# Optimization experiments

Measured on AMD Instinct MI355X. Metric: run time of the kernel, lower is better.

Reference implementation:

```python
import jax, jax.numpy as jnp
import numpy as np

# quantization / activation scales (stand-ins for act_scales dict entries)
S_IN = 0.05      # in_proj:input
S_Z = 0.02       # in_proj:output (also gate/z scale)
S_U = 0.01       # x_proj:input (conv output scale)
S_DTLN = 0.02    # dt_layernorm:output
S_B = 0.02       # B_layernorm:output
S_C = 0.02       # C_layernorm:output
S_DT = 0.01      # dt_proj:output
S_Y = 0.01       # out_proj:input
EPS = 1e-6
R = 128          # time_step_rank
N = 16           # ssm_state_size


def qa(x, s):
    # simulate int8 activation quantization (values kept in fp32)
    return jnp.clip(jnp.round(x / s), -128.0, 127.0)


def qw(w):
    # per-tensor symmetric int8 weight quantization
    s = jnp.max(jnp.abs(w)) / 127.0
    return jnp.clip(jnp.round(w / s), -128.0, 127.0), s


def rmsnorm_q(x, w, s):
    x = x.astype(jnp.float32)
    x = x * jax.lax.rsqrt(jnp.mean(x * x, axis=-1, keepdims=True) + EPS)
    return qa(w * x, s)


def ssm_scan(u, dt, A, Bm, Cm):
    # u, dt: [B, D, S]; Bm, Cm: [B, S, N]; A: [D, N]
    def step(h, xs):
        dt_t, u_t, B_t, C_t = xs                     # [B,D],[B,D],[B,N],[B,N]
        dA = jnp.exp(dt_t[..., None] * A)            # [B,D,N]
        h = h * dA + (dt_t * u_t)[..., None] * B_t[:, None, :]
        y = jnp.einsum('bdn,bn->bd', h, C_t)
        return h, y
    Bsz, Dd, S = u.shape
    h0 = jnp.zeros((Bsz, Dd, A.shape[1]), u.dtype)
    xs = (jnp.moveaxis(dt, 2, 0), jnp.moveaxis(u, 2, 0),
          jnp.moveaxis(Bm, 1, 0), jnp.moveaxis(Cm, 1, 0))
    _, ys = jax.lax.scan(step, h0, xs)               # ys: [S,B,D]
    return jnp.moveaxis(ys, 0, 2)                    # [B,D,S]


def setup_inputs() -> dict:
    key = jax.random.key(0)
    ks = jax.random.split(key, 10)
    B, S, H, Din, K = 2, 2048, 2048, 4096, 4
    return {
        'hidden_states': jax.random.normal(ks[0], (B, S, H), jnp.float32),
        'in_proj_w': jax.random.normal(ks[1], (2 * Din, H), jnp.float32) * 0.02,
        'conv_w': jax.random.normal(ks[2], (Din, K), jnp.float32) * 0.1,
        'conv_b': jax.random.normal(ks[3], (Din,), jnp.float32) * 0.01,
        'x_proj_w': jax.random.normal(ks[4], (R + 2 * N, Din), jnp.float32) * 0.02,
        'dt_ln_w': jnp.ones((R,), jnp.float32),
        'B_ln_w': jnp.ones((N,), jnp.float32),
        'C_ln_w': jnp.ones((N,), jnp.float32),
        'dt_proj_w': jax.random.normal(ks[5], (Din, R), jnp.float32) * 0.05,
        'dt_bias': jax.random.normal(ks[6], (Din,), jnp.float32) * 0.5 - 4.0,
        'A_log': jnp.log(jnp.broadcast_to(jnp.arange(1, N + 1, dtype=jnp.float32), (Din, N))),
        'D_skip': jnp.ones((Din,), jnp.float32),
        'out_proj_w': jax.random.normal(ks[7], (H, Din), jnp.float32) * 0.02,
    }


def reference(hidden_states, in_proj_w, conv_w, conv_b, x_proj_w, dt_ln_w,
              B_ln_w, C_ln_w, dt_proj_w, dt_bias, A_log, D_skip, out_proj_w):
    # --- in_proj (W8A8B8O8), then seqlen-last layout [B, 2D, S] ---
    x_q = qa(hidden_states, S_IN)
    wq, ws = qw(in_proj_w)
    proj_q = qa((x_q @ wq.T) * (S_IN * ws), S_Z)          # [B,S,2D] int8-valued
    proj_q = jnp.swapaxes(proj_q, 1, 2)                   # [B,2D,S]
    Din = proj_q.shape[1] // 2
    hs_q, gate_q = proj_q[:, :Din], proj_q[:, Din:]

    # --- quantized causal depthwise conv1d + silu (QCausalConv1D) ---
    cwq, cws = qw(conv_w)
    K = conv_w.shape[1]
    conv_out = jax.lax.conv_general_dilated(
        hs_q, cwq[:, None, :], (1,), [(K - 1, 0)],
        dimension_numbers=('NCH', 'OIH', 'NCH'), feature_group_count=Din)
    conv_out = conv_out * (S_Z * cws) + conv_b[None, :, None]
    u_q = qa(jax.nn.silu(conv_out), S_U)                  # [B,Din,S]

    # --- x_proj (W8A8BF16OF16) -> dt/B/C, inner RMSNorms + quant ---
    xwq, xws = qw(x_proj_w)
    ssm_p = (jnp.swapaxes(u_q, 1, 2) @ xwq.T) * (S_U * xws)   # [B,S,R+2N] float
    dt_q = rmsnorm_q(ssm_p[..., :R], dt_ln_w, S_DTLN)
    B_q = rmsnorm_q(ssm_p[..., R:R + N], B_ln_w, S_B)
    C_q = rmsnorm_q(ssm_p[..., R + N:], C_ln_w, S_C)

    # --- dt_proj (W8A8B8O8, bias folded into scan) ---
    dwq, dws = qw(dt_proj_w)
    dt8 = qa((dt_q @ dwq.T) * (S_DTLN * dws), S_DT)       # [B,S,Din]
    dt = jax.nn.softplus(jnp.swapaxes(dt8, 1, 2) * S_DT + dt_bias[None, :, None])

    # --- selective scan (QSScan): dequantize, recur, gate ---
    u = u_q * S_U
    A = -jnp.exp(A_log)
    ys = ssm_scan(u, dt, A, B_q * S_B, C_q * S_C)         # [B,Din,S]
    ys = ys + u * D_skip[None, :, None]
    ys = ys * jax.nn.silu(gate_q * S_Z)

    # --- QAct + out_proj (W8A8BF16OF16) ---
    y_q = qa(jnp.swapaxes(ys, 1, 2), S_Y)                 # [B,S,Din]
    owq, ows = qw(out_proj_w)
    return (y_q @ owq.T) * (S_Y * ows)                    # [B,S,H]
```

## Files before the change

### kernel.cpp

```cpp
#include <hip/hip_runtime.h>
#include <stdint.h>

typedef signed char i8;
typedef int v4i __attribute__((ext_vector_type(4)));

#define S_IN  0.05f
#define S_Z   0.02f
#define S_U   0.01f
#define S_DTLN 0.02f
#define S_B   0.02f
#define S_C   0.02f
#define S_DT  0.01f
#define S_Y   0.01f

__device__ __forceinline__ float q8f(float x, float s) {
    float r = rintf(x / s);
    return fmaxf(-128.0f, fminf(127.0f, r));
}
__device__ __forceinline__ int q8i(float x, float s) { return (int)q8f(x, s); }

__device__ __forceinline__ float softplus_f(float x) {
    return __fadd_rn(fmaxf(x, 0.0f), log1pf(expf(-fabsf(x))));
}

__device__ __forceinline__ int sbyte_of(int w, int j) {
    return (int)(signed char)((unsigned)w >> (j * 8));
}
__device__ __forceinline__ int ubyte_of(int w, int j) {
    return (int)(((unsigned)w >> (j * 8)) & 255u);
}

__device__ __forceinline__ void gload16(const i8* g, i8* lds) {
    __builtin_amdgcn_global_load_lds(
        (const __attribute__((address_space(1))) unsigned int*)g,
        (__attribute__((address_space(3))) unsigned int*)lds,
        16, 0, 0);
}

__global__ __launch_bounds__(256)
void k_maxabs_all(const float* __restrict__ a0, const float* __restrict__ a1,
                  const float* __restrict__ a2, const float* __restrict__ a3,
                  const float* __restrict__ a4, unsigned* __restrict__ out) {
    int bid = blockIdx.x;
    const float* w; long long n; int slot, nb;
    if (bid < 2048)      { w = a0; n = 16777216LL; slot = 0; nb = 2048; }
    else if (bid < 2112) { w = a1; n = 16384LL;    slot = 1; nb = 64;   bid -= 2048; }
    else if (bid < 2624) { w = a2; n = 655360LL;   slot = 2; nb = 512;  bid -= 2112; }
    else if (bid < 3136) { w = a3; n = 524288LL;   slot = 3; nb = 512;  bid -= 2624; }
    else                 { w = a4; n = 8388608LL;  slot = 4; nb = 1024; bid -= 3136; }
    unsigned m = 0;
    long long stride = (long long)nb * 256;
    for (long long i = (long long)bid * 256 + threadIdx.x; i < n; i += stride)
        m = max(m, __float_as_uint(fabsf(w[i])));
    #pragma unroll
    for (int off = 32; off; off >>= 1) {
        unsigned o = (unsigned)__shfl_xor((int)m, off);
        m = max(m, o);
    }
    __shared__ unsigned sm[4];
    if ((threadIdx.x & 63) == 0) sm[threadIdx.x >> 6] = m;
    __syncthreads();
    if (threadIdx.x == 0) {
        unsigned r = max(max(sm[0], sm[1]), max(sm[2], sm[3]));
        atomicMax(out + slot, r);
    }
}

__global__ __launch_bounds__(256)
void k_quant_all(const float* __restrict__ a0, const float* __restrict__ a1,
                 const float* __restrict__ a2, const float* __restrict__ a3,
                 const float* __restrict__ a4, const float* __restrict__ ax,
                 const unsigned* __restrict__ scales,
                 i8* __restrict__ o0, i8* __restrict__ o1, i8* __restrict__ o2,
                 i8* __restrict__ o3, i8* __restrict__ o4, i8* __restrict__ ox) {
    int bid = blockIdx.x;
    const float* w; i8* o; float s;
    if (bid < 16384)      { w = a0; o = o0; s = __uint_as_float(scales[0]) / 127.0f; }
    else if (bid < 16400) { w = a1; o = o1; s = __uint_as_float(scales[1]) / 127.0f; bid -= 16384; }
    else if (bid < 17040) { w = a2; o = o2; s = __uint_as_float(scales[2]) / 127.0f; bid -= 16400; }
    else if (bid < 17552) { w = a3; o = o3; s = __uint_as_float(scales[3]) / 127.0f; bid -= 17040; }
    else if (bid < 25744) { w = a4; o = o4; s = __uint_as_float(scales[4]) / 127.0f; bid -= 17552; }
    else                  { w = ax; o = ox; s = S_IN;                                 bid -= 25744; }
    long long i = ((long long)bid * 256 + threadIdx.x) * 4;
    float4 v = *(const float4*)(w + i);
    unsigned pk = ((unsigned)(q8i(v.x, s) & 255))
                | ((unsigned)(q8i(v.y, s) & 255) << 8)
                | ((unsigned)(q8i(v.z, s) & 255) << 16)
                | ((unsigned)(q8i(v.w, s) & 255) << 24);
    *(unsigned*)(o + i) = pk;
}

template<int EPI>
__global__ __launch_bounds__(256)
void k_mgemm(const i8* __restrict__ A, const i8* __restrict__ Bw,
             int M, int N, int K,
             const unsigned* __restrict__ wmaxbits,
             void* __restrict__ out0, void* __restrict__ out1) {
    __shared__ i8 sA[16384];
    __shared__ i8 sB[16384];
    const int tid = threadIdx.x;
    const int w = tid >> 6;
    const int l = tid & 63;
    int id = blockIdx.y * gridDim.x + blockIdx.x;
    const int qq = (gridDim.x * gridDim.y) >> 3;
    id = (id & 7) * qq + (id >> 3);
    const int m0 = (id / gridDim.x) << 7;
    const int n0 = (id % gridDim.x) << 7;
    const int kLen = K / gridDim.z;
    const int kOff = blockIdx.z * kLen;
    const int lr = l & 15;
    const int lk = l >> 4;
    const i8* gA = A  + (size_t)(m0 + lr) * K + lk * 16;
    const i8* gB = Bw + (size_t)(n0 + lr) * K + lk * 16;
    const size_t rowK16 = (size_t)16 * K;
    const int mw = (w >> 1) * 4;
    const int nw = (w & 1) * 4;
    const int rdoff = lk * 256 + lr * 16;
    v4i acc[4][4] = {};
    for (int k0 = kOff; k0 < kOff + kLen; k0 += 128) {
        gload16(gA + rowK16 * w + k0,            sA + w * 2048);
        gload16(gA + rowK16 * w + k0 + 64,       sA + w * 2048 + 1024);
        gload16(gA + rowK16 * (4 + w) + k0,      sA + (4 + w) * 2048);
        gload16(gA + rowK16 * (4 + w) + k0 + 64, sA + (4 + w) * 2048 + 1024);
        gload16(gB + rowK16 * w + k0,            sB + w * 2048);
        gload16(gB + rowK16 * w + k0 + 64,       sB + w * 2048 + 1024);
        gload16(gB + rowK16 * (4 + w) + k0,      sB + (4 + w) * 2048);
        gload16(gB + rowK16 * (4 + w) + k0 + 64, sB + (4 + w) * 2048 + 1024);
        __syncthreads();
        #pragma unroll
        for (int k64 = 0; k64 < 2; k64++) {
            v4i af[4], bf[4];
            #pragma unroll
            for (int t = 0; t < 4; t++) {
                af[t] = *(const v4i*)(sA + (mw + t) * 2048 + k64 * 1024 + rdoff);
                bf[t] = *(const v4i*)(sB + (nw + t) * 2048 + k64 * 1024 + rdoff);
            }
            #pragma unroll
            for (int mt = 0; mt < 4; mt++)
                #pragma unroll
                for (int nt = 0; nt < 4; nt++)
                    acc[mt][nt] = __builtin_amdgcn_mfma_i32_16x16x64_i8(af[mt], bf[nt], acc[mt][nt], 0, 0, 0);
        }
        __syncthreads();
    }
    const float wsc = __uint_as_float(*wmaxbits) / 127.0f;
    const int m0w = m0 + (w >> 1) * 64;
    const int n0w = n0 + (w & 1) * 64;
    if constexpr (EPI == 0 || EPI == 2) {
        const float sc = (EPI == 0 ? S_IN : S_DTLN) * wsc;
        const float qs = (EPI == 0 ? S_Z : S_DT);
        const int b = m0w >> 11;
        #pragma unroll
        for (int nt = 0; nt < 4; nt++) {
            const int j = n0w + nt * 16 + lr;
            i8* dst;
            if constexpr (EPI == 0) dst = (j < 4096) ? (i8*)out0 : (i8*)out1;
            else dst = (i8*)out0;
            const int jj = j & 4095;
            #pragma unroll
            for (int mt = 0; mt < 4; mt++) {
                const int sbase = (m0w & 2047) + mt * 16 + lk * 4;
                unsigned pk = 0;
                #pragma unroll
                for (int r = 0; r < 4; r++) {
                    float v = (float)acc[mt][nt][r] * sc;
                    pk |= ((unsigned)(q8i(v, qs) & 255)) << (8 * r);
                }
                *(unsigned*)(dst + ((size_t)b * 4096 + jj) * 2048 + sbase) = pk;
            }
        }
    } else if constexpr (EPI == 1) {
        int* O = (int*)out0;
        #pragma unroll
        for (int mt = 0; mt < 4; mt++)
            #pragma unroll
            for (int r = 0; r < 4; r++) {
                const int m = m0w + mt * 16 + lk * 4 + r;
                #pragma unroll
                for (int nt = 0; nt < 4; nt++) {
                    const int j = n0w + nt * 16 + lr;
                    if (j < 160)
                        atomicAdd(O + (size_t)m * 160 + j, acc[mt][nt][r]);
                }
            }
    } else {
        const float sc = S_Y * wsc;
        float* O = (float*)out0;
        #pragma unroll
        for (int mt = 0; mt < 4; mt++)
            #pragma unroll
            for (int r = 0; r < 4; r++) {
                const int m = m0w + mt * 16 + lk * 4 + r;
                #pragma unroll
                for (int nt = 0; nt < 4; nt++)
                    O[(size_t)m * N + n0w + nt * 16 + lr] = (float)acc[mt][nt][r] * sc;
            }
    }
}

__global__ __launch_bounds__(256)
void k_conv(const i8* __restrict__ hsq, const i8* __restrict__ cwq,
            const float* __restrict__ conv_b, const unsigned* __restrict__ cmaxbits,
            i8* __restrict__ uq, i8* __restrict__ uqT) {
    __shared__ char lt[64][68];
    const int tid = threadIdx.x;
    const int b = blockIdx.z;
    const int d0 = blockIdx.y << 6;
    const int s0 = blockIdx.x << 6;
    const int dl = tid >> 2;
    const int sg = tid & 3;
    const int d = d0 + dl;
    const int sbase = s0 + (sg << 4);
    const i8* xp = hsq + ((size_t)b * 4096 + d) * 2048;
    int v[19];
    #pragma unroll
    for (int i = 0; i < 19; i++) {
        int s = sbase - 3 + i;
        v[i] = (s >= 0) ? (int)xp[s] : 0;
    }
    const unsigned cw = *(const unsigned*)(cwq + (size_t)d * 4);
    const int w0 = (int)(char)(cw & 255);
    const int w1 = (int)(char)((cw >> 8) & 255);
    const int w2 = (int)(char)((cw >> 16) & 255);
    const int w3 = (int)(char)((cw >> 24) & 255);
    const float cws = __uint_as_float(*cmaxbits) / 127.0f;
    const float sc = S_Z * cws;
    const float bias = conv_b[d];
    unsigned pk[4] = {0, 0, 0, 0};
    #pragma unroll
    for (int t = 0; t < 16; t++) {
        int acc = v[t] * w0 + v[t + 1] * w1 + v[t + 2] * w2 + v[t + 3] * w3;
        float f = __fadd_rn(__fmul_rn((float)acc, sc), bias);
        float sig = 1.0f / (1.0f + expf(-f));
        float sl = __fmul_rn(f, sig);
        int q = q8i(sl, S_U);
        pk[t >> 2] |= ((unsigned)(q & 255)) << ((t & 3) * 8);
        lt[(sg << 4) + t][dl] = (char)q;
    }
    *(int4*)(uq + ((size_t)b * 4096 + d) * 2048 + sbase) = make_int4(pk[0], pk[1], pk[2], pk[3]);
    __syncthreads();
    const int rr = tid >> 2;
    const int wg = tid & 3;
    const int* rp = (const int*)(&lt[rr][wg << 4]);
    int4 o; o.x = rp[0]; o.y = rp[1]; o.z = rp[2]; o.w = rp[3];
    *(int4*)(uqT + ((size_t)b * 2048 + s0 + rr) * 4096 + d0 + (wg << 4)) = o;
}

__global__ __launch_bounds__(64)
void k_rms(const int* __restrict__ p, const unsigned* __restrict__ xsc,
           const float* __restrict__ wdt, const float* __restrict__ wB, const float* __restrict__ wC,
           i8* __restrict__ dtq, i8* __restrict__ bqT, i8* __restrict__ cqT) {
    const int row = blockIdx.x;
    const int lane = threadIdx.x;
    const float scp = S_U * (__uint_as_float(*xsc) / 127.0f);
    const int* x = p + (size_t)row * 160;
    float a0 = (float)x[lane] * scp;
    float a1 = (float)x[64 + lane] * scp;
    float bb = (lane < 16) ? (float)x[128 + lane] * scp : 0.0f;
    float cc = (lane < 16) ? (float)x[144 + lane] * scp : 0.0f;
    float sdt = __fadd_rn(__fmul_rn(a0, a0), __fmul_rn(a1, a1));
    float sB = __fmul_rn(bb, bb);
    float sC = __fmul_rn(cc, cc);
    #pragma unroll
    for (int off = 32; off; off >>= 1) {
        sdt = __fadd_rn(sdt, __shfl_xor(sdt, off));
        sB  = __fadd_rn(sB,  __shfl_xor(sB, off));
        sC  = __fadd_rn(sC,  __shfl_xor(sC, off));
    }
    float rdt = 1.0f / sqrtf(sdt / 128.0f + 1e-6f);
    float rB  = 1.0f / sqrtf(sB / 16.0f + 1e-6f);
    float rC  = 1.0f / sqrtf(sC / 16.0f + 1e-6f);
    dtq[(size_t)row * 128 + lane]      = (i8)q8i(__fmul_rn(wdt[lane],      __fmul_rn(a0, rdt)), S_DTLN);
    dtq[(size_t)row * 128 + 64 + lane] = (i8)q8i(__fmul_rn(wdt[64 + lane], __fmul_rn(a1, rdt)), S_DTLN);
    if (lane < 16) {
        size_t tpos = ((size_t)(row >> 11) * 16 + lane) * 2048 + (row & 2047);
        bqT[tpos] = (i8)q8i(__fmul_rn(wB[lane], __fmul_rn(bb, rB)), S_B);
        cqT[tpos] = (i8)q8i(__fmul_rn(wC[lane], __fmul_rn(cc, rC)), S_C);
    }
}

__global__ __launch_bounds__(256)
void k_lut_all(const float* __restrict__ dt_bias, float* __restrict__ lutdt,
               float* __restrict__ lutsi) {
    const int q = threadIdx.x;
    const int sv = (q < 128) ? q : q - 256;
    if (blockIdx.x < 4096) {
        const int d = blockIdx.x;
        const float bias = dt_bias[d];
        lutdt[(size_t)d * 256 + q] =
            softplus_f(__fadd_rn(__fmul_rn((float)sv, S_DT), bias));
    } else {
        float gv = __fmul_rn((float)sv, S_Z);
        float sg = __fmul_rn(gv, 1.0f / (1.0f + expf(-gv)));
        lutsi[q] = sg;
    }
}

__global__ __launch_bounds__(256)
void k_scan4(const i8* __restrict__ dt8, const i8* __restrict__ uq, const i8* __restrict__ gq,
             const i8* __restrict__ BqT, const i8* __restrict__ CqT,
             const float* __restrict__ lut_dt, const float* __restrict__ lut_silu,
             const float* __restrict__ A_log, const float* __restrict__ D_skip,
             i8* __restrict__ yq) {
    const int g = blockIdx.x * 256 + threadIdx.x;
    const int n = g & 15;
    const int bd = g >> 4;
    const int d = bd & 4095;
    const int b = bd >> 12;
    const float Acoef = -expf(A_log[(size_t)d * 16 + n]);
    const float Dd = D_skip[d];
    const float* ldt = lut_dt + (size_t)d * 256;
    const v4i* dtp = (const v4i*)(dt8 + (size_t)bd * 2048);
    const v4i* up  = (const v4i*)(uq  + (size_t)bd * 2048);
    const v4i* gp  = (const v4i*)(gq  + (size_t)bd * 2048);
    const v4i* Bp  = (const v4i*)(BqT + ((size_t)b * 16 + n) * 2048);
    const v4i* Cp  = (const v4i*)(CqT + ((size_t)b * 16 + n) * 2048);
    i8* yp = yq + (size_t)b * 2048 * 4096 + d;
    float h = 0.0f;
    v4i dtw = dtp[0], uw = up[0], gw = gp[0], bw = Bp[0], cw = Cp[0];
    for (int t = 0; t < 128; t++) {
        v4i ndt, nu, ng, nb, nc;
        if (t < 127) { ndt = dtp[t + 1]; nu = up[t + 1]; ng = gp[t + 1]; nb = Bp[t + 1]; nc = Cp[t + 1]; }
        float dtv[16], dA[16], pj[16], Cv[16], y[16];
        #pragma unroll
        for (int j = 0; j < 16; j++)
            dtv[j] = ldt[ubyte_of(dtw[j >> 2], j & 3)];
        #pragma unroll
        for (int j = 0; j < 16; j++)
            dA[j] = expf(__fmul_rn(dtv[j], Acoef));
        #pragma unroll
        for (int j = 0; j < 16; j++) {
            float uv = __fmul_rn((float)sbyte_of(uw[j >> 2], j & 3), S_U);
            float Bv = __fmul_rn((float)sbyte_of(bw[j >> 2], j & 3), S_B);
            Cv[j] = __fmul_rn((float)sbyte_of(cw[j >> 2], j & 3), S_C);
            pj[j] = __fmul_rn(__fmul_rn(dtv[j], uv), Bv);
        }
        #pragma unroll
        for (int j = 0; j < 16; j++) {
            h = __fadd_rn(__fmul_rn(h, dA[j]), pj[j]);
            y[j] = __fmul_rn(h, Cv[j]);
        }
        float w8[8];
        #pragma unroll
        for (int i = 0; i < 8; i++) {
            float a = y[2 * i], bq = y[2 * i + 1];
            float snd = (n & 1) ? a : bq;
            float rcv = __shfl_xor(snd, 1);
            float kept = (n & 1) ? bq : a;
            w8[i] = __fadd_rn(kept, rcv);
        }
        float w4[4];
        #pragma unroll
        for (int i = 0; i < 4; i++) {
            float a = w8[2 * i], bq = w8[2 * i + 1];
            float snd = (n & 2) ? a : bq;
            float rcv = __shfl_xor(snd, 2);
            float kept = (n & 2) ? bq : a;
            w4[i] = __fadd_rn(kept, rcv);
        }
        float w2[2];
        #pragma unroll
        for (int i = 0; i < 2; i++) {
            float a = w4[2 * i], bq = w4[2 * i + 1];
            float snd = (n & 4) ? a : bq;
            float rcv = __shfl_xor(snd, 4);
            float kept = (n & 4) ? bq : a;
            w2[i] = __fadd_rn(kept, rcv);
        }
        float ysave;
        {
            float a = w2[0], bq = w2[1];
            float snd = (n & 8) ? a : bq;
            float rcv = __shfl_xor(snd, 8);
            float kept = (n & 8) ? bq : a;
            ysave = __fadd_rn(kept, rcv);
        }
        int uws = (n & 8) ? ((n & 4) ? uw[3] : uw[2]) : ((n & 4) ? uw[1] : uw[0]);
        int gws = (n & 8) ? ((n & 4) ? gw[3] : gw[2]) : ((n & 4) ? gw[1] : gw[0]);
        float uvn = __fmul_rn((float)(int)(signed char)((unsigned)uws >> ((n & 3) * 8)), S_U);
        int gb = (int)(((unsigned)gws >> ((n & 3) * 8)) & 255u);
        float ys = __fadd_rn(ysave, __fmul_rn(uvn, Dd));
        float sg = lut_silu[gb];
        float vv = __fmul_rn(ys, sg);
        yp[(size_t)(t * 16 + n) * 4096] = (i8)q8i(vv, S_Y);
        if (t < 127) { dtw = ndt; uw = nu; gw = ng; bw = nb; cw = nc; }
    }
}

extern "C" void kernel_launch(void* const* d_in, const int* in_sizes, int n_in,
                              void* d_out, int out_size, void* d_ws, size_t ws_size,
                              hipStream_t stream) {
    const float* hidden   = (const float*)d_in[0];
    const float* in_proj  = (const float*)d_in[1];
    const float* conv_w   = (const float*)d_in[2];
    const float* conv_b   = (const float*)d_in[3];
    const float* x_proj   = (const float*)d_in[4];
    const float* dt_ln    = (const float*)d_in[5];
    const float* B_ln     = (const float*)d_in[6];
    const float* C_ln     = (const float*)d_in[7];
    const float* dt_proj  = (const float*)d_in[8];
    const float* dt_bias  = (const float*)d_in[9];
    const float* A_log    = (const float*)d_in[10];
    const float* D_skip   = (const float*)d_in[11];
    const float* out_proj = (const float*)d_in[12];
    float* out = (float*)d_out;

    char* ws = (char*)d_ws;
    unsigned* scales = (unsigned*)ws;
    i8* WQ   = (i8*)(ws + 256);
    i8* XQ   = (i8*)(ws + 16777472);
    i8* HSQ  = (i8*)(ws + 25166080);
    char* S0 = ws + 41943296;
    int*  SSMP = (int*)S0;
    i8* XWQp = (i8*)(S0 + 2621440);
    i8* DTQb = (i8*)(S0 + 3670016);
    i8* DWQ  = (i8*)(S0 + 4194304);
    i8* CWQ  = (i8*)(S0 + 4718592);
    float* LUTSI = (float*)(S0 + 4734976);
    i8* BQT  = (i8*)(S0 + 4736000);
    i8* CQT  = (i8*)(S0 + 4801536);
    float* LUTDT = (float*)S0;
    i8* OWQ  = (i8*)(ws + 46810368);

    i8* GQ = (i8*)d_out;
    i8* UQ = (i8*)d_out + 16777216;
    i8* UQT = WQ;
    i8* DT8 = HSQ;
    i8* YQ  = WQ;

    hipMemsetAsync(scales, 0, 256, stream);
    hipMemsetAsync(SSMP, 0, 2621440, stream);
    hipMemsetAsync(XWQp, 0, 1048576, stream);

    k_maxabs_all<<<4160, 256, 0, stream>>>(in_proj, conv_w, x_proj, dt_proj, out_proj, scales);

    k_quant_all<<<33936, 256, 0, stream>>>(in_proj, conv_w, x_proj, dt_proj, out_proj, hidden,
                                           scales, WQ, CWQ, XWQp, DWQ, OWQ, XQ);

    k_mgemm<0><<<dim3(64, 32), 256, 0, stream>>>(XQ, WQ, 4096, 8192, 2048, scales + 0, HSQ, GQ);

    dim3 gc(32, 64, 2);
    k_conv<<<gc, 256, 0, stream>>>(HSQ, CWQ, conv_b, scales + 1, UQ, UQT);

    k_mgemm<1><<<dim3(2, 32, 8), 256, 0, stream>>>(UQT, XWQp, 4096, 256, 4096, scales + 2, SSMP, nullptr);

    k_rms<<<4096, 64, 0, stream>>>(SSMP, scales + 2, dt_ln, B_ln, C_ln, DTQb, BQT, CQT);

    k_mgemm<2><<<dim3(32, 32), 256, 0, stream>>>(DTQb, DWQ, 4096, 4096, 128, scales + 3, DT8, nullptr);

    k_lut_all<<<4097, 256, 0, stream>>>(dt_bias, LUTDT, LUTSI);

    k_scan4<<<512, 256, 0, stream>>>(DT8, UQ, GQ, BQT, CQT, LUTDT, LUTSI, A_log, D_skip, YQ);

    k_mgemm<3><<<dim3(16, 32), 256, 0, stream>>>(YQ, OWQ, 4096, 2048, 4096, scales + 4, out, nullptr);
}
```

Measured before the change: 656.1 us.

## Add 256x256-tile double-buffered int8 GEMM for in_proj and out_proj

Introduces a new 512-thread int8 MFMA GEMM kernel with 256x256 output tiles, double-buffered shared memory with explicit waitcnt, block-id swizzling for L2 locality, and wave priority boosting around the MFMA block. It replaces the 128x128 kernel for the two large GEMMs (in_proj and out_proj), and the old kernel's epilogues are trimmed to the remaining uses. Larger tiles raise arithmetic intensity and the prefetch overlaps global loads with compute. The cost is more registers per thread (8x4 accumulators) and fewer blocks, so occupancy and tail effects could suffer.

```diff
diff --git a/kernel.cpp b/kernel.cpp
--- a/kernel.cpp
+++ b/kernel.cpp
@@ -146,30 +146,7 @@
     const float wsc = __uint_as_float(*wmaxbits) / 127.0f;
     const int m0w = m0 + (w >> 1) * 64;
     const int n0w = n0 + (w & 1) * 64;
-    if constexpr (EPI == 0 || EPI == 2) {
-        const float sc = (EPI == 0 ? S_IN : S_DTLN) * wsc;
-        const float qs = (EPI == 0 ? S_Z : S_DT);
-        const int b = m0w >> 11;
-        #pragma unroll
-        for (int nt = 0; nt < 4; nt++) {
-            const int j = n0w + nt * 16 + lr;
-            i8* dst;
-            if constexpr (EPI == 0) dst = (j < 4096) ? (i8*)out0 : (i8*)out1;
-            else dst = (i8*)out0;
-            const int jj = j & 4095;
-            #pragma unroll
-            for (int mt = 0; mt < 4; mt++) {
-                const int sbase = (m0w & 2047) + mt * 16 + lk * 4;
-                unsigned pk = 0;
-                #pragma unroll
-                for (int r = 0; r < 4; r++) {
-                    float v = (float)acc[mt][nt][r] * sc;
-                    pk |= ((unsigned)(q8i(v, qs) & 255)) << (8 * r);
-                }
-                *(unsigned*)(dst + ((size_t)b * 4096 + jj) * 2048 + sbase) = pk;
-            }
-        }
-    } else if constexpr (EPI == 1) {
+    if constexpr (EPI == 1) {
         int* O = (int*)out0;
         #pragma unroll
         for (int mt = 0; mt < 4; mt++)
@@ -184,10 +161,123 @@
                 }
             }
     } else {
+        const float sc = S_DTLN * wsc;
+        const int b = m0w >> 11;
+        i8* dst = (i8*)out0;
+        #pragma unroll
+        for (int nt = 0; nt < 4; nt++) {
+            const int j = n0w + nt * 16 + lr;
+            #pragma unroll
+            for (int mt = 0; mt < 4; mt++) {
+                const int sbase = (m0w & 2047) + mt * 16 + lk * 4;
+                unsigned pk = 0;
+                #pragma unroll
+                for (int r = 0; r < 4; r++) {
+                    float v = (float)acc[mt][nt][r] * sc;
+                    pk |= ((unsigned)(q8i(v, S_DT) & 255)) << (8 * r);
+                }
+                *(unsigned*)(dst + ((size_t)b * 4096 + j) * 2048 + sbase) = pk;
+            }
+        }
+    }
+}
+
+template<int EPI>
+__global__ __launch_bounds__(512)
+void k_mg2(const i8* __restrict__ A, const i8* __restrict__ Bw,
+           int M, int N, int K,
+           const unsigned* __restrict__ wmaxbits,
+           void* __restrict__ out0, void* __restrict__ out1) {
+    __shared__ i8 sA[2][16384];
+    __shared__ i8 sB[2][16384];
+    const int tid = threadIdx.x;
+    const int w = tid >> 6;
+    const int l = tid & 63;
+    const int lr = l & 15;
+    const int lk = l >> 4;
+    int id = blockIdx.y * gridDim.x + blockIdx.x;
+    const int qq = (gridDim.x * gridDim.y) >> 3;
+    id = (id & 7) * qq + (id >> 3);
+    const int m0 = (id / gridDim.x) << 8;
+    const int n0 = (id % gridDim.x) << 8;
+    const int wr = w >> 2;
+    const int wc = w & 3;
+    const i8* gA0 = A  + (size_t)(m0 + w * 16 + lr) * K + lk * 16;
+    const i8* gA1 = A  + (size_t)(m0 + (8 + w) * 16 + lr) * K + lk * 16;
+    const i8* gB0 = Bw + (size_t)(n0 + w * 16 + lr) * K + lk * 16;
+    const i8* gB1 = Bw + (size_t)(n0 + (8 + w) * 16 + lr) * K + lk * 16;
+    const int rdoff = lk * 256 + lr * 16;
+    v4i acc[8][4] = {};
+    const int NT = K >> 6;
+    gload16(gA0, sA[0] + w * 1024);
+    gload16(gA1, sA[0] + (8 + w) * 1024);
+    gload16(gB0, sB[0] + w * 1024);
+    gload16(gB1, sB[0] + (8 + w) * 1024);
+    int cur = 0;
+    for (int kt = 0; kt < NT; kt++) {
+        if (kt + 1 < NT) {
+            const int k1 = (kt + 1) << 6;
+            i8* dA = (cur ? sA[0] : sA[1]);
+            i8* dB = (cur ? sB[0] : sB[1]);
+            gload16(gA0 + k1, dA + w * 1024);
+            gload16(gA1 + k1, dA + (8 + w) * 1024);
+            gload16(gB0 + k1, dB + w * 1024);
+            gload16(gB1 + k1, dB + (8 + w) * 1024);
+            asm volatile("s_waitcnt vmcnt(4)" ::: "memory");
+        } else {
+            asm volatile("s_waitcnt vmcnt(0)" ::: "memory");
+        }
+        __builtin_amdgcn_s_barrier();
+        __builtin_amdgcn_sched_barrier(0);
+        const i8* rA = (cur ? sA[1] : sA[0]);
+        const i8* rB = (cur ? sB[1] : sB[0]);
+        v4i af[8], bf[4];
+        #pragma unroll
+        for (int t = 0; t < 8; t++)
+            af[t] = *(const v4i*)(rA + (wr * 8 + t) * 1024 + rdoff);
+        #pragma unroll
+        for (int t = 0; t < 4; t++)
+            bf[t] = *(const v4i*)(rB + (wc * 4 + t) * 1024 + rdoff);
+        __builtin_amdgcn_s_setprio(1);
+        #pragma unroll
+        for (int mt = 0; mt < 8; mt++)
+            #pragma unroll
+            for (int nt = 0; nt < 4; nt++)
+                acc[mt][nt] = __builtin_amdgcn_mfma_i32_16x16x64_i8(af[mt], bf[nt], acc[mt][nt], 0, 0, 0);
+        __builtin_amdgcn_s_setprio(0);
+        __builtin_amdgcn_sched_barrier(0);
+        __builtin_amdgcn_s_barrier();
+        __builtin_amdgcn_sched_barrier(0);
+        cur ^= 1;
+    }
+    const float wsc = __uint_as_float(*wmaxbits) / 127.0f;
+    const int m0w = m0 + wr * 128;
+    const int n0w = n0 + wc * 64;
+    if constexpr (EPI == 0) {
+        const float sc = S_IN * wsc;
+        const int b = m0w >> 11;
+        #pragma unroll
+        for (int nt = 0; nt < 4; nt++) {
+            const int j = n0w + nt * 16 + lr;
+            i8* dst = (j < 4096) ? (i8*)out0 : (i8*)out1;
+            const int jj = j & 4095;
+            #pragma unroll
+            for (int mt = 0; mt < 8; mt++) {
+                const int sbase = (m0w & 2047) + mt * 16 + lk * 4;
+                unsigned pk = 0;
+                #pragma unroll
+                for (int r = 0; r < 4; r++) {
+                    float v = (float)acc[mt][nt][r] * sc;
+                    pk |= ((unsigned)(q8i(v, S_Z) & 255)) << (8 * r);
+                }
+                *(unsigned*)(dst + ((size_t)b * 4096 + jj) * 2048 + sbase) = pk;
+            }
+        }
+    } else {
         const float sc = S_Y * wsc;
         float* O = (float*)out0;
         #pragma unroll
-        for (int mt = 0; mt < 4; mt++)
+        for (int mt = 0; mt < 8; mt++)
             #pragma unroll
             for (int r = 0; r < 4; r++) {
                 const int m = m0w + mt * 16 + lk * 4 + r;
@@ -437,7 +527,7 @@
     k_quant_all<<<33936, 256, 0, stream>>>(in_proj, conv_w, x_proj, dt_proj, out_proj, hidden,
                                            scales, WQ, CWQ, XWQp, DWQ, OWQ, XQ);
 
-    k_mgemm<0><<<dim3(64, 32), 256, 0, stream>>>(XQ, WQ, 4096, 8192, 2048, scales + 0, HSQ, GQ);
+    k_mg2<0><<<dim3(32, 16), 512, 0, stream>>>(XQ, WQ, 4096, 8192, 2048, scales + 0, HSQ, GQ);
 
     dim3 gc(32, 64, 2);
     k_conv<<<gc, 256, 0, stream>>>(HSQ, CWQ, conv_b, scales + 1, UQ, UQT);
@@ -446,11 +536,11 @@
 
     k_rms<<<4096, 64, 0, stream>>>(SSMP, scales + 2, dt_ln, B_ln, C_ln, DTQb, BQT, CQT);
 
-    k_mgemm<2><<<dim3(32, 32), 256, 0, stream>>>(DTQb, DWQ, 4096, 4096, 128, scales + 3, DT8, nullptr);
+    k_mgemm<2><<<dim3(32, 32, 1), 256, 0, stream>>>(DTQb, DWQ, 4096, 4096, 128, scales + 3, DT8, nullptr);
 
     k_lut_all<<<4097, 256, 0, stream>>>(dt_bias, LUTDT, LUTSI);
 
     k_scan4<<<512, 256, 0, stream>>>(DT8, UQ, GQ, BQT, CQT, LUTDT, LUTSI, A_log, D_skip, YQ);
 
-    k_mgemm<3><<<dim3(16, 32), 256, 0, stream>>>(YQ, OWQ, 4096, 2048, 4096, scales + 4, out, nullptr);
-}
+    k_mg2<3><<<dim3(8, 16), 512, 0, stream>>>(YQ, OWQ, 4096, 2048, 4096, scales + 4, out, nullptr);
+}
```

Result: slower. 674.0 us (+2.7%).
